# Performance work log

Measured on AMD Instinct MI355X. Metric: run time of the kernel, lower is better.

The kernel has to match this reference:

```python
import jax, jax.numpy as jnp
import numpy as np
import math

DIM_IN, DIM_CTX, DIM_KEY, DIM_VAL = 2048, 512, 128, 128
N, T, H, W = 8, 16, 32, 32
NBOX = 512


def setup_inputs() -> dict:
    key = jax.random.key(0)
    ks = jax.random.split(key, 10)
    rois = jax.random.normal(ks[0], (NBOX, DIM_IN), dtype=jnp.float32)
    context = jax.random.normal(ks[1], (N, DIM_CTX, T, H, W), dtype=jnp.float32)
    batch_idx = jnp.sort(jax.random.randint(ks[2], (NBOX,), 0, N))
    s = 0.02
    W_proj = jax.random.normal(ks[3], (DIM_KEY, DIM_IN), dtype=jnp.float32) * s
    b_proj = jnp.zeros((DIM_KEY,), dtype=jnp.float32)
    W_keys = jax.random.normal(ks[4], (DIM_KEY, DIM_CTX), dtype=jnp.float32) * s
    b_keys = jnp.zeros((DIM_KEY,), dtype=jnp.float32)
    W_vals = jax.random.normal(ks[5], (DIM_VAL, DIM_CTX), dtype=jnp.float32) * s
    b_vals = jnp.zeros((DIM_VAL,), dtype=jnp.float32)
    return {"rois": rois, "context": context, "batch_idx": batch_idx,
            "W_proj": W_proj, "b_proj": b_proj,
            "W_keys": W_keys, "b_keys": b_keys,
            "W_vals": W_vals, "b_vals": b_vals}


def reference(rois, context, batch_idx, W_proj, b_proj, W_keys, b_keys, W_vals, b_vals):
    n, c, t, h, w = context.shape
    s = t * h * w
    dk = W_keys.shape[0]
    # ROI query projection: [Nb, dk]
    q = rois @ W_proj.T + b_proj
    # 1x1x1 Conv3d == per-voxel linear over channels
    ctx_flat = context.reshape(n, c, s)                       # [N, C, S]
    keys = jnp.einsum('kc,ncs->nks', W_keys, ctx_flat) + b_keys[None, :, None]  # [N, dk, S]
    vals = jnp.einsum('vc,ncs->nsv', W_vals, ctx_flat) + b_vals[None, None, :]  # [N, S, dv]
    # Per-box gather of its clip's keys/vals, fused cross-attention
    qk = jnp.einsum('bk,bks->bs', q, keys[batch_idx]) / math.sqrt(dk)  # [Nb, S]
    coeff = jax.nn.softmax(qk, axis=-1)
    ctx_out = jnp.einsum('bs,bsv->bv', coeff, vals[batch_idx])         # [Nb, dv]
    attn = coeff.reshape(-1, t, h, w) * 255.0
    return ctx_out, attn
```

## Files before the change

kernel.cpp:

```cpp
#include <hip/hip_runtime.h>
#include <hip/hip_bf16.h>
#include <math.h>

#define DIM_IN  2048
#define DIM_CTX 512
#define DIM_KEY 128
#define DIM_VAL 128
#define NCLIP   8
#define S_TOT   16384
#define NBOX    512
#define MAXB    96

typedef __attribute__((ext_vector_type(8))) short short8_t;
typedef __attribute__((ext_vector_type(4))) float f32x4;

__device__ inline unsigned short f2bf(float x) {
    union { float f; unsigned int u; } v; v.f = x;
    unsigned int r = v.u + 0x7FFFu + ((v.u >> 16) & 1u);
    return (unsigned short)(r >> 16);
}
__device__ inline float bf2f(unsigned short h) {
    union { unsigned int u; float f; } v; v.u = ((unsigned int)h) << 16;
    return v.f;
}

__global__ __launch_bounds__(256) void k0_init(const int* __restrict__ batch_idx,
                                               int* __restrict__ ranges,
                                               float* __restrict__ cctx) {
    int idx = blockIdx.x * blockDim.x + threadIdx.x;
    for (int i = idx; i < NBOX * DIM_CTX; i += gridDim.x * blockDim.x)
        cctx[i] = 0.0f;
    if (blockIdx.x == 0) {
        __shared__ int s_start[NCLIP], s_end[NCLIP];
        if (threadIdx.x < NCLIP) { s_start[threadIdx.x] = NBOX; s_end[threadIdx.x] = 0; }
        __syncthreads();
        for (int i = threadIdx.x; i < NBOX; i += blockDim.x) {
            int b = batch_idx[i];
            atomicMin(&s_start[b], i);
            atomicMax(&s_end[b], i + 1);
        }
        __syncthreads();
        if (threadIdx.x < NCLIP) {
            ranges[threadIdx.x]         = s_start[threadIdx.x];
            ranges[NCLIP + threadIdx.x] = s_end[threadIdx.x];
        }
    }
}

__global__ __launch_bounds__(128) void k1a_q(const float* __restrict__ rois,
                                             const float* __restrict__ W_proj,
                                             const float* __restrict__ b_proj,
                                             float* __restrict__ q) {
    __shared__ float s_roi[4 * DIM_IN];
    int b0 = blockIdx.x * 4;
    const float4* src = (const float4*)(rois + (size_t)b0 * DIM_IN);
    for (int i = threadIdx.x; i < 4 * DIM_IN / 4; i += blockDim.x)
        ((float4*)s_roi)[i] = src[i];
    __syncthreads();
    int k = threadIdx.x;
    const float4* wrow = (const float4*)(W_proj + (size_t)k * DIM_IN);
    float a0 = 0.f, a1 = 0.f, a2 = 0.f, a3 = 0.f;
    for (int i = 0; i < DIM_IN / 4; ++i) {
        float4 w  = wrow[i];
        float4 r0 = *(const float4*)&s_roi[0 * DIM_IN + i * 4];
        float4 r1 = *(const float4*)&s_roi[1 * DIM_IN + i * 4];
        float4 r2 = *(const float4*)&s_roi[2 * DIM_IN + i * 4];
        float4 r3 = *(const float4*)&s_roi[3 * DIM_IN + i * 4];
        a0 += w.x * r0.x; a0 += w.y * r0.y; a0 += w.z * r0.z; a0 += w.w * r0.w;
        a1 += w.x * r1.x; a1 += w.y * r1.y; a1 += w.z * r1.z; a1 += w.w * r1.w;
        a2 += w.x * r2.x; a2 += w.y * r2.y; a2 += w.z * r2.z; a2 += w.w * r2.w;
        a3 += w.x * r3.x; a3 += w.y * r3.y; a3 += w.z * r3.z; a3 += w.w * r3.w;
    }
    float bp = b_proj[k];
    q[(size_t)(b0 + 0) * DIM_KEY + k] = a0 + bp;
    q[(size_t)(b0 + 1) * DIM_KEY + k] = a1 + bp;
    q[(size_t)(b0 + 2) * DIM_KEY + k] = a2 + bp;
    q[(size_t)(b0 + 3) * DIM_KEY + k] = a3 + bp;
}

__global__ __launch_bounds__(256) void k1b_qw(const float* __restrict__ q,
                                              const float* __restrict__ W_keys,
                                              const float* __restrict__ b_keys,
                                              unsigned short* __restrict__ qW_hi,
                                              unsigned short* __restrict__ qW_lo,
                                              float* __restrict__ qbias) {
    __shared__ float s_q[4 * DIM_KEY];
    __shared__ float red[256];
    int b0 = blockIdx.x * 4;
    for (int i = threadIdx.x; i < 4 * DIM_KEY; i += blockDim.x)
        s_q[i] = q[(size_t)b0 * DIM_KEY + i];
    __syncthreads();
    int c0 = threadIdx.x, c1 = threadIdx.x + 256;
    float a[4][2] = {{0.f,0.f},{0.f,0.f},{0.f,0.f},{0.f,0.f}};
    for (int k = 0; k < DIM_KEY; ++k) {
        float w0 = W_keys[(size_t)k * DIM_CTX + c0];
        float w1 = W_keys[(size_t)k * DIM_CTX + c1];
        float q0 = s_q[0 * DIM_KEY + k], q1 = s_q[1 * DIM_KEY + k];
        float q2 = s_q[2 * DIM_KEY + k], q3 = s_q[3 * DIM_KEY + k];
        a[0][0] += q0 * w0; a[0][1] += q0 * w1;
        a[1][0] += q1 * w0; a[1][1] += q1 * w1;
        a[2][0] += q2 * w0; a[2][1] += q2 * w1;
        a[3][0] += q3 * w0; a[3][1] += q3 * w1;
    }
    #pragma unroll
    for (int j = 0; j < 4; ++j) {
        #pragma unroll
        for (int cc = 0; cc < 2; ++cc) {
            int c = (cc == 0) ? c0 : c1;
            float x = a[j][cc];
            unsigned short h = f2bf(x);
            qW_hi[(size_t)(b0 + j) * DIM_CTX + c] = h;
            qW_lo[(size_t)(b0 + j) * DIM_CTX + c] = f2bf(x - bf2f(h));
        }
    }
    for (int j = 0; j < 4; ++j) {
        float v = 0.f;
        if (threadIdx.x < DIM_KEY) v = s_q[j * DIM_KEY + threadIdx.x] * b_keys[threadIdx.x];
        red[threadIdx.x] = v;
        __syncthreads();
        for (int st = 128; st > 0; st >>= 1) {
            if (threadIdx.x < st) red[threadIdx.x] += red[threadIdx.x + st];
            __syncthreads();
        }
        if (threadIdx.x == 0) qbias[b0 + j] = red[0];
        __syncthreads();
    }
}

__global__ __launch_bounds__(256) void k2_scores(
    const float* __restrict__ ctx, const unsigned short* __restrict__ qW_hi,
    const unsigned short* __restrict__ qW_lo, const float* __restrict__ qbias,
    const int* __restrict__ ranges, float* __restrict__ scores)
{
    int n = blockIdx.y;
    int start = ranges[n], Mb = ranges[NCLIP + n] - start;
    if (Mb <= 0) return;
    const float* ctxn = ctx + (size_t)n * DIM_CTX * S_TOT;
    int sch = blockIdx.x * 128;
    int t = threadIdx.x, lane = t & 63, w = t >> 6;

    __shared__ float          ls_f[32 * 132];
    __shared__ unsigned short ls_qh[MAXB * 32];
    __shared__ unsigned short ls_ql[MAXB * 32];
    __shared__ unsigned short ls_th[128 * 32];
    __shared__ unsigned short ls_tl[128 * 32];

    for (int bp = 0; bp < Mb; bp += MAXB) {
        int nb = min(MAXB, Mb - bp);
        f32x4 acc[6][2];
        #pragma unroll
        for (int m = 0; m < 6; ++m)
            #pragma unroll
            for (int nn = 0; nn < 2; ++nn)
                acc[m][nn] = (f32x4){0.f, 0.f, 0.f, 0.f};

        for (int ch = 0; ch < 16; ++ch) {
            int c0 = ch * 32;
            __syncthreads();
            #pragma unroll
            for (int rep = 0; rep < 4; ++rep) {
                int idx = t + rep * 256;
                int c_l = idx >> 5, s4 = (idx & 31) * 4;
                float4 v = *(const float4*)(ctxn + (size_t)(c0 + c_l) * S_TOT + sch + s4);
                *(float4*)&ls_f[c_l * 132 + s4] = v;
            }
            for (int idx = t; idx < MAXB * 4; idx += 256) {
                int row = idx >> 2, c8 = (idx & 3) * 8;
                uint4 vh = {0,0,0,0}, vl = {0,0,0,0};
                if (row < nb) {
                    size_t go = (size_t)(start + bp + row) * DIM_CTX + c0 + c8;
                    vh = *(const uint4*)(qW_hi + go);
                    vl = *(const uint4*)(qW_lo + go);
                }
                int off = (row * 64 + c8 * 2) ^ ((row & 7) << 4);
                *(uint4*)((char*)ls_qh + off) = vh;
                *(uint4*)((char*)ls_ql + off) = vl;
            }
            __syncthreads();
            {
                int s_l = t >> 1, c16 = (t & 1) * 16;
                unsigned short hb[16], lb[16];
                #pragma unroll
                for (int i = 0; i < 16; ++i) {
                    float x = ls_f[(c16 + i) * 132 + s_l];
                    unsigned short h = f2bf(x);
                    hb[i] = h;
                    lb[i] = f2bf(x - bf2f(h));
                }
                int base = s_l * 64 + c16 * 2;
                int sw = (s_l & 7) << 4;
                uint4 p0, p1, q0, q1;
                p0.x = hb[0] | ((unsigned)hb[1] << 16);  p0.y = hb[2] | ((unsigned)hb[3] << 16);
                p0.z = hb[4] | ((unsigned)hb[5] << 16);  p0.w = hb[6] | ((unsigned)hb[7] << 16);
                p1.x = hb[8] | ((unsigned)hb[9] << 16);  p1.y = hb[10] | ((unsigned)hb[11] << 16);
                p1.z = hb[12] | ((unsigned)hb[13] << 16); p1.w = hb[14] | ((unsigned)hb[15] << 16);
                q0.x = lb[0] | ((unsigned)lb[1] << 16);  q0.y = lb[2] | ((unsigned)lb[3] << 16);
                q0.z = lb[4] | ((unsigned)lb[5] << 16);  q0.w = lb[6] | ((unsigned)lb[7] << 16);
                q1.x = lb[8] | ((unsigned)lb[9] << 16);  q1.y = lb[10] | ((unsigned)lb[11] << 16);
                q1.z = lb[12] | ((unsigned)lb[13] << 16); q1.w = lb[14] | ((unsigned)lb[15] << 16);
                *(uint4*)((char*)ls_th + ((base)      ^ sw)) = p0;
                *(uint4*)((char*)ls_th + ((base + 16) ^ sw)) = p1;
                *(uint4*)((char*)ls_tl + ((base)      ^ sw)) = q0;
                *(uint4*)((char*)ls_tl + ((base + 16) ^ sw)) = q1;
            }
            __syncthreads();
            short8_t Ah[6], Al[6], Bh[2], Bl[2];
            int hi16 = (lane >> 4) * 16;
            #pragma unroll
            for (int m = 0; m < 6; ++m) {
                if (m * 16 < nb) {
                    int row = m * 16 + (lane & 15);
                    int off = (row * 64 + hi16) ^ ((row & 7) << 4);
                    Ah[m] = *(const short8_t*)((const char*)ls_qh + off);
                    Al[m] = *(const short8_t*)((const char*)ls_ql + off);
                }
            }
            #pragma unroll
            for (int nn = 0; nn < 2; ++nn) {
                int srow = (w * 2 + nn) * 16 + (lane & 15);
                int off = (srow * 64 + hi16) ^ ((srow & 7) << 4);
                Bh[nn] = *(const short8_t*)((const char*)ls_th + off);
                Bl[nn] = *(const short8_t*)((const char*)ls_tl + off);
            }
            #pragma unroll
            for (int m = 0; m < 6; ++m) {
                if (m * 16 < nb) {
                    #pragma unroll
                    for (int nn = 0; nn < 2; ++nn) {
                        acc[m][nn] = __builtin_amdgcn_mfma_f32_16x16x32_bf16(Ah[m], Bh[nn], acc[m][nn], 0, 0, 0);
                        acc[m][nn] = __builtin_amdgcn_mfma_f32_16x16x32_bf16(Ah[m], Bl[nn], acc[m][nn], 0, 0, 0);
                        acc[m][nn] = __builtin_amdgcn_mfma_f32_16x16x32_bf16(Al[m], Bh[nn], acc[m][nn], 0, 0, 0);
                    }
                }
            }
        }
        const float rs = 0.08838834764831845f;
        #pragma unroll
        for (int m = 0; m < 6; ++m)
            #pragma unroll
            for (int r = 0; r < 4; ++r) {
                int b_l = m * 16 + ((lane >> 4) << 2) + r;
                if (b_l < nb) {
                    int bg = start + bp + b_l;
                    float qb = qbias[bg];
                    #pragma unroll
                    for (int nn = 0; nn < 2; ++nn) {
                        int s = sch + (w * 2 + nn) * 16 + (lane & 15);
                        scores[(size_t)bg * S_TOT + s] = (acc[m][nn][r] + qb) * rs;
                    }
                }
            }
        __syncthreads();
    }
}

__global__ __launch_bounds__(256) void k3_stats(const float* __restrict__ scores,
                                                float* __restrict__ rmax,
                                                float* __restrict__ rsum) {
    int b = blockIdx.x;
    const float4* row = (const float4*)(scores + (size_t)b * S_TOT);
    __shared__ float red[256];
    float mx = -1e30f;
    for (int i = threadIdx.x; i < S_TOT / 4; i += 256) {
        float4 v = row[i];
        mx = fmaxf(mx, fmaxf(fmaxf(v.x, v.y), fmaxf(v.z, v.w)));
    }
    red[threadIdx.x] = mx;
    __syncthreads();
    for (int st = 128; st > 0; st >>= 1) {
        if (threadIdx.x < st) red[threadIdx.x] = fmaxf(red[threadIdx.x], red[threadIdx.x + st]);
        __syncthreads();
    }
    mx = red[0];
    __syncthreads();
    float sm = 0.f;
    for (int i = threadIdx.x; i < S_TOT / 4; i += 256) {
        float4 v = row[i];
        sm += __expf(v.x - mx) + __expf(v.y - mx) + __expf(v.z - mx) + __expf(v.w - mx);
    }
    red[threadIdx.x] = sm;
    __syncthreads();
    for (int st = 128; st > 0; st >>= 1) {
        if (threadIdx.x < st) red[threadIdx.x] += red[threadIdx.x + st];
        __syncthreads();
    }
    if (threadIdx.x == 0) { rmax[b] = mx; rsum[b] = 1.0f / red[0]; }
}

__global__ __launch_bounds__(256) void k4_pv(
    const float* __restrict__ ctx, const int* __restrict__ ranges,
    const float* __restrict__ rmax, const float* __restrict__ rsum,
    float* __restrict__ attn, float* __restrict__ cctx)
{
    int n = blockIdx.y;
    int start = ranges[n], Mb = ranges[NCLIP + n] - start;
    if (Mb <= 0) return;
    const float* ctxn = ctx + (size_t)n * DIM_CTX * S_TOT;
    int sch = blockIdx.x * 256;
    int t = threadIdx.x, lane = t & 63, w = t >> 6;
    int mh = w >> 1, ns = w & 1;

    __shared__ unsigned short ls_p[MAXB * 256];
    __shared__ unsigned short ls_c[32 * 256];

    for (int bp = 0; bp < Mb; bp += MAXB) {
        int nb = min(MAXB, Mb - bp);
        bool a0v = (mh + 0) * 16 < nb;
        bool a1v = (mh + 2) * 16 < nb;
        bool a2v = (mh + 4) * 16 < nb;
        __syncthreads();
        for (int idx = t; idx < MAXB * 64; idx += 256) {
            int b_l = idx >> 6, s4 = (idx & 63) * 4;
            uint2 pk; pk.x = 0u; pk.y = 0u;
            if (b_l < nb) {
                int bg = start + bp + b_l;
                size_t off = (size_t)bg * S_TOT + sch + s4;
                float4 v = *(const float4*)(attn + off);
                float m = rmax[bg], r = rsum[bg];
                float4 p;
                p.x = __expf(v.x - m) * r; p.y = __expf(v.y - m) * r;
                p.z = __expf(v.z - m) * r; p.w = __expf(v.w - m) * r;
                float4 o;
                o.x = 255.f * p.x; o.y = 255.f * p.y; o.z = 255.f * p.z; o.w = 255.f * p.w;
                *(float4*)(attn + off) = o;
                pk.x = f2bf(p.x) | ((unsigned)f2bf(p.y) << 16);
                pk.y = f2bf(p.z) | ((unsigned)f2bf(p.w) << 16);
            }
            int off8 = (b_l * 512 + s4 * 2) ^ ((b_l & 7) << 4);
            *(uint2*)((char*)ls_p + off8) = pk;
        }
        __syncthreads();
        short8_t A[3][8];
        int hi16 = (lane >> 4) * 16;
        #pragma unroll
        for (int mi = 0; mi < 3; ++mi) {
            int tm = mh + 2 * mi;
            if (tm * 16 < nb) {
                int row = tm * 16 + (lane & 15);
                int sw = (row & 7) << 4;
                #pragma unroll
                for (int k = 0; k < 8; ++k) {
                    int off = (row * 512 + k * 64 + hi16) ^ sw;
                    A[mi][k] = *(const short8_t*)((const char*)ls_p + off);
                }
            }
        }
        for (int ct = 0; ct < 16; ++ct) {
            __syncthreads();
            for (int idx = t; idx < 32 * 64; idx += 256) {
                int c_l = idx >> 6, s4 = (idx & 63) * 4;
                float4 v = *(const float4*)(ctxn + (size_t)(ct * 32 + c_l) * S_TOT + sch + s4);
                uint2 pk;
                pk.x = f2bf(v.x) | ((unsigned)f2bf(v.y) << 16);
                pk.y = f2bf(v.z) | ((unsigned)f2bf(v.w) << 16);
                int off8 = (c_l * 512 + s4 * 2) ^ ((c_l & 7) << 4);
                *(uint2*)((char*)ls_c + off8) = pk;
            }
            __syncthreads();
            f32x4 acc0 = (f32x4){0,0,0,0}, acc1 = (f32x4){0,0,0,0}, acc2 = (f32x4){0,0,0,0};
            int crow = ns * 16 + (lane & 15);
            int swc = (crow & 7) << 4;
            #pragma unroll
            for (int k = 0; k < 8; ++k) {
                int off = (crow * 512 + k * 64 + hi16) ^ swc;
                short8_t B = *(const short8_t*)((const char*)ls_c + off);
                if (a0v) acc0 = __builtin_amdgcn_mfma_f32_16x16x32_bf16(A[0][k], B, acc0, 0, 0, 0);
                if (a1v) acc1 = __builtin_amdgcn_mfma_f32_16x16x32_bf16(A[1][k], B, acc1, 0, 0, 0);
                if (a2v) acc2 = __builtin_amdgcn_mfma_f32_16x16x32_bf16(A[2][k], B, acc2, 0, 0, 0);
            }
            int cg = ct * 32 + ns * 16 + (lane & 15);
            #pragma unroll
            for (int r = 0; r < 4; ++r) {
                int br = ((lane >> 4) << 2) + r;
                int b0l = (mh + 0) * 16 + br;
                int b1l = (mh + 2) * 16 + br;
                int b2l = (mh + 4) * 16 + br;
                if (a0v && b0l < nb) atomicAdd(&cctx[(size_t)(start + bp + b0l) * DIM_CTX + cg], acc0[r]);
                if (a1v && b1l < nb) atomicAdd(&cctx[(size_t)(start + bp + b1l) * DIM_CTX + cg], acc1[r]);
                if (a2v && b2l < nb) atomicAdd(&cctx[(size_t)(start + bp + b2l) * DIM_CTX + cg], acc2[r]);
            }
        }
    }
}

__global__ __launch_bounds__(128) void k5_out(const float* __restrict__ cctx,
                                              const float* __restrict__ W_vals,
                                              const float* __restrict__ b_vals,
                                              float* __restrict__ out) {
    __shared__ float s_c[4 * DIM_CTX];
    int b0 = blockIdx.x * 4;
    const float4* src = (const float4*)(cctx + (size_t)b0 * DIM_CTX);
    for (int i = threadIdx.x; i < 4 * DIM_CTX / 4; i += blockDim.x)
        ((float4*)s_c)[i] = src[i];
    __syncthreads();
    int v = threadIdx.x;
    const float4* wrow = (const float4*)(W_vals + (size_t)v * DIM_CTX);
    float a0 = 0.f, a1 = 0.f, a2 = 0.f, a3 = 0.f;
    for (int i = 0; i < DIM_CTX / 4; ++i) {
        float4 w  = wrow[i];
        float4 c0v = *(const float4*)&s_c[0 * DIM_CTX + i * 4];
        float4 c1v = *(const float4*)&s_c[1 * DIM_CTX + i * 4];
        float4 c2v = *(const float4*)&s_c[2 * DIM_CTX + i * 4];
        float4 c3v = *(const float4*)&s_c[3 * DIM_CTX + i * 4];
        a0 += w.x * c0v.x; a0 += w.y * c0v.y; a0 += w.z * c0v.z; a0 += w.w * c0v.w;
        a1 += w.x * c1v.x; a1 += w.y * c1v.y; a1 += w.z * c1v.z; a1 += w.w * c1v.w;
        a2 += w.x * c2v.x; a2 += w.y * c2v.y; a2 += w.z * c2v.z; a2 += w.w * c2v.w;
        a3 += w.x * c3v.x; a3 += w.y * c3v.y; a3 += w.z * c3v.z; a3 += w.w * c3v.w;
    }
    float bb = b_vals[v];
    out[(size_t)(b0 + 0) * DIM_VAL + v] = a0 + bb;
    out[(size_t)(b0 + 1) * DIM_VAL + v] = a1 + bb;
    out[(size_t)(b0 + 2) * DIM_VAL + v] = a2 + bb;
    out[(size_t)(b0 + 3) * DIM_VAL + v] = a3 + bb;
}

extern "C" void kernel_launch(void* const* d_in, const int* in_sizes, int n_in,
                              void* d_out, int out_size, void* d_ws, size_t ws_size,
                              hipStream_t stream) {
    const float* rois      = (const float*)d_in[0];
    const float* context   = (const float*)d_in[1];
    const int*   batch_idx = (const int*)  d_in[2];
    const float* W_proj    = (const float*)d_in[3];
    const float* b_proj    = (const float*)d_in[4];
    const float* W_keys    = (const float*)d_in[5];
    const float* b_keys    = (const float*)d_in[6];
    const float* W_vals    = (const float*)d_in[7];
    const float* b_vals    = (const float*)d_in[8];

    float* out  = (float*)d_out;
    float* attn = out + NBOX * DIM_VAL;

    char* wsb = (char*)d_ws;
    int*   ranges = (int*)wsb;
    float* q      = (float*)(wsb + 128);
    float* qbias  = q + NBOX * DIM_KEY;
    float* rmaxp  = qbias + NBOX;
    float* rsump  = rmaxp + NBOX;
    float* cctx   = rsump + NBOX;
    unsigned short* qW_hi = (unsigned short*)(cctx + NBOX * DIM_CTX);
    unsigned short* qW_lo = qW_hi + NBOX * DIM_CTX;

    k0_init  <<<dim3(64),       dim3(256), 0, stream>>>(batch_idx, ranges, cctx);
    k1a_q    <<<dim3(NBOX / 4), dim3(128), 0, stream>>>(rois, W_proj, b_proj, q);
    k1b_qw   <<<dim3(NBOX / 4), dim3(256), 0, stream>>>(q, W_keys, b_keys, qW_hi, qW_lo, qbias);
    k2_scores<<<dim3(128, 8),   dim3(256), 0, stream>>>(context, qW_hi, qW_lo, qbias, ranges, attn);
    k3_stats <<<dim3(NBOX),     dim3(256), 0, stream>>>(attn, rmaxp, rsump);
    k4_pv    <<<dim3(64, 8),    dim3(256), 0, stream>>>(context, ranges, rmaxp, rsump, attn, cctx);
    k5_out   <<<dim3(NBOX / 4), dim3(128), 0, stream>>>(cctx, W_vals, b_vals, out);
}
```

Before: 645.7 us.

## Precompute bf16 context copies once, drop low-part split for scores

Adds a conversion kernel that reads the fp32 context once and writes both a channel-major bf16 copy and a transposed voxel-major bf16 copy. The scores kernel then loads pre-transposed bf16 tiles directly and drops the per-block fp32->bf16 hi/lo split, using two MFMA products instead of three. The PV kernel reads the bf16 copy instead of converting fp32. This removes repeated conversion work and halves context read bytes in the consumers, at the cost of an extra full pass writing 32MB of bf16 data and lower score precision on the context side.

```diff
diff --git a/kernel.cpp b/kernel.cpp
--- a/kernel.cpp
+++ b/kernel.cpp
@@ -45,6 +45,42 @@
             ranges[NCLIP + threadIdx.x] = s_end[threadIdx.x];
         }
     }
+}
+
+__global__ __launch_bounds__(256) void conv_ctx(const float* __restrict__ ctx,
+                                                unsigned short* __restrict__ ctxB,
+                                                unsigned short* __restrict__ ctxT) {
+    int n = blockIdx.z;
+    int c0 = blockIdx.y * 64;
+    int sch = blockIdx.x * 128;
+    int t = threadIdx.x;
+    __shared__ float ls[64 * 132];
+    const float* src = ctx + ((size_t)n * DIM_CTX + c0) * S_TOT + sch;
+    unsigned short* dstB = ctxB + ((size_t)n * DIM_CTX + c0) * S_TOT + sch;
+    #pragma unroll
+    for (int r = 0; r < 8; ++r) {
+        int idx = t + r * 256;
+        int c_l = idx >> 5, s4 = (idx & 31) * 4;
+        float4 v = *(const float4*)(src + (size_t)c_l * S_TOT + s4);
+        *(float4*)&ls[c_l * 132 + s4] = v;
+        uint2 pk;
+        pk.x = f2bf(v.x) | ((unsigned)f2bf(v.y) << 16);
+        pk.y = f2bf(v.z) | ((unsigned)f2bf(v.w) << 16);
+        *(uint2*)(dstB + (size_t)c_l * S_TOT + s4) = pk;
+    }
+    __syncthreads();
+    int s_l = t >> 1, ch = (t & 1) * 32;
+    unsigned int pk[16];
+    #pragma unroll
+    for (int i = 0; i < 16; ++i) {
+        unsigned short h0 = f2bf(ls[(ch + 2 * i + 0) * 132 + s_l]);
+        unsigned short h1 = f2bf(ls[(ch + 2 * i + 1) * 132 + s_l]);
+        pk[i] = h0 | ((unsigned)h1 << 16);
+    }
+    unsigned short* dstT = ctxT + ((size_t)n * S_TOT + sch + s_l) * DIM_CTX + c0 + ch;
+    #pragma unroll
+    for (int i = 0; i < 4; ++i)
+        ((uint4*)dstT)[i] = *(uint4*)&pk[i * 4];
 }
 
 __global__ __launch_bounds__(128) void k1a_q(const float* __restrict__ rois,
@@ -128,22 +164,20 @@
 }
 
 __global__ __launch_bounds__(256) void k2_scores(
-    const float* __restrict__ ctx, const unsigned short* __restrict__ qW_hi,
+    const unsigned short* __restrict__ ctxT, const unsigned short* __restrict__ qW_hi,
     const unsigned short* __restrict__ qW_lo, const float* __restrict__ qbias,
     const int* __restrict__ ranges, float* __restrict__ scores)
 {
     int n = blockIdx.y;
     int start = ranges[n], Mb = ranges[NCLIP + n] - start;
     if (Mb <= 0) return;
-    const float* ctxn = ctx + (size_t)n * DIM_CTX * S_TOT;
+    const unsigned short* ctxTn = ctxT + (size_t)n * S_TOT * DIM_CTX;
     int sch = blockIdx.x * 128;
     int t = threadIdx.x, lane = t & 63, w = t >> 6;
 
-    __shared__ float          ls_f[32 * 132];
-    __shared__ unsigned short ls_qh[MAXB * 32];
-    __shared__ unsigned short ls_ql[MAXB * 32];
-    __shared__ unsigned short ls_th[128 * 32];
-    __shared__ unsigned short ls_tl[128 * 32];
+    __shared__ unsigned short ls_b[128 * 64];
+    __shared__ unsigned short ls_qh[MAXB * 64];
+    __shared__ unsigned short ls_ql[MAXB * 64];
 
     for (int bp = 0; bp < Mb; bp += MAXB) {
         int nb = min(MAXB, Mb - bp);
@@ -154,82 +188,56 @@
             for (int nn = 0; nn < 2; ++nn)
                 acc[m][nn] = (f32x4){0.f, 0.f, 0.f, 0.f};
 
-        for (int ch = 0; ch < 16; ++ch) {
-            int c0 = ch * 32;
+        for (int it = 0; it < 8; ++it) {
+            int c0 = it * 64;
             __syncthreads();
             #pragma unroll
-            for (int rep = 0; rep < 4; ++rep) {
-                int idx = t + rep * 256;
-                int c_l = idx >> 5, s4 = (idx & 31) * 4;
-                float4 v = *(const float4*)(ctxn + (size_t)(c0 + c_l) * S_TOT + sch + s4);
-                *(float4*)&ls_f[c_l * 132 + s4] = v;
-            }
-            for (int idx = t; idx < MAXB * 4; idx += 256) {
-                int row = idx >> 2, c8 = (idx & 3) * 8;
+            for (int r = 0; r < 4; ++r) {
+                int idx = t + r * 256;
+                int s_l = idx >> 3, c8 = (idx & 7) * 8;
+                uint4 v = *(const uint4*)(ctxTn + (size_t)(sch + s_l) * DIM_CTX + c0 + c8);
+                *(uint4*)((char*)ls_b + ((s_l * 128 + c8 * 2) ^ ((s_l & 7) << 4))) = v;
+            }
+            for (int idx = t; idx < MAXB * 8; idx += 256) {
+                int row = idx >> 3, c8 = (idx & 7) * 8;
                 uint4 vh = {0,0,0,0}, vl = {0,0,0,0};
                 if (row < nb) {
                     size_t go = (size_t)(start + bp + row) * DIM_CTX + c0 + c8;
                     vh = *(const uint4*)(qW_hi + go);
                     vl = *(const uint4*)(qW_lo + go);
                 }
-                int off = (row * 64 + c8 * 2) ^ ((row & 7) << 4);
+                int off = (row * 128 + c8 * 2) ^ ((row & 7) << 4);
                 *(uint4*)((char*)ls_qh + off) = vh;
                 *(uint4*)((char*)ls_ql + off) = vl;
             }
             __syncthreads();
-            {
-                int s_l = t >> 1, c16 = (t & 1) * 16;
-                unsigned short hb[16], lb[16];
+            #pragma unroll
+            for (int ks = 0; ks < 2; ++ks) {
+                int hi16 = ks * 64 + (lane >> 4) * 16;
+                short8_t Ah[6], Al[6], Bv[2];
                 #pragma unroll
-                for (int i = 0; i < 16; ++i) {
-                    float x = ls_f[(c16 + i) * 132 + s_l];
-                    unsigned short h = f2bf(x);
-                    hb[i] = h;
-                    lb[i] = f2bf(x - bf2f(h));
-                }
-                int base = s_l * 64 + c16 * 2;
-                int sw = (s_l & 7) << 4;
-                uint4 p0, p1, q0, q1;
-                p0.x = hb[0] | ((unsigned)hb[1] << 16);  p0.y = hb[2] | ((unsigned)hb[3] << 16);
-                p0.z = hb[4] | ((unsigned)hb[5] << 16);  p0.w = hb[6] | ((unsigned)hb[7] << 16);
-                p1.x = hb[8] | ((unsigned)hb[9] << 16);  p1.y = hb[10] | ((unsigned)hb[11] << 16);
-                p1.z = hb[12] | ((unsigned)hb[13] << 16); p1.w = hb[14] | ((unsigned)hb[15] << 16);
-                q0.x = lb[0] | ((unsigned)lb[1] << 16);  q0.y = lb[2] | ((unsigned)lb[3] << 16);
-                q0.z = lb[4] | ((unsigned)lb[5] << 16);  q0.w = lb[6] | ((unsigned)lb[7] << 16);
-                q1.x = lb[8] | ((unsigned)lb[9] << 16);  q1.y = lb[10] | ((unsigned)lb[11] << 16);
-                q1.z = lb[12] | ((unsigned)lb[13] << 16); q1.w = lb[14] | ((unsigned)lb[15] << 16);
-                *(uint4*)((char*)ls_th + ((base)      ^ sw)) = p0;
-                *(uint4*)((char*)ls_th + ((base + 16) ^ sw)) = p1;
-                *(uint4*)((char*)ls_tl + ((base)      ^ sw)) = q0;
-                *(uint4*)((char*)ls_tl + ((base + 16) ^ sw)) = q1;
-            }
-            __syncthreads();
-            short8_t Ah[6], Al[6], Bh[2], Bl[2];
-            int hi16 = (lane >> 4) * 16;
-            #pragma unroll
-            for (int m = 0; m < 6; ++m) {
-                if (m * 16 < nb) {
-                    int row = m * 16 + (lane & 15);
-                    int off = (row * 64 + hi16) ^ ((row & 7) << 4);
-                    Ah[m] = *(const short8_t*)((const char*)ls_qh + off);
-                    Al[m] = *(const short8_t*)((const char*)ls_ql + off);
-                }
-            }
-            #pragma unroll
-            for (int nn = 0; nn < 2; ++nn) {
-                int srow = (w * 2 + nn) * 16 + (lane & 15);
-                int off = (srow * 64 + hi16) ^ ((srow & 7) << 4);
-                Bh[nn] = *(const short8_t*)((const char*)ls_th + off);
-                Bl[nn] = *(const short8_t*)((const char*)ls_tl + off);
-            }
-            #pragma unroll
-            for (int m = 0; m < 6; ++m) {
-                if (m * 16 < nb) {
-                    #pragma unroll
-                    for (int nn = 0; nn < 2; ++nn) {
-                        acc[m][nn] = __builtin_amdgcn_mfma_f32_16x16x32_bf16(Ah[m], Bh[nn], acc[m][nn], 0, 0, 0);
-                        acc[m][nn] = __builtin_amdgcn_mfma_f32_16x16x32_bf16(Ah[m], Bl[nn], acc[m][nn], 0, 0, 0);
-                        acc[m][nn] = __builtin_amdgcn_mfma_f32_16x16x32_bf16(Al[m], Bh[nn], acc[m][nn], 0, 0, 0);
+                for (int m = 0; m < 6; ++m) {
+                    if (m * 16 < nb) {
+                        int row = m * 16 + (lane & 15);
+                        int off = (row * 128 + hi16) ^ ((row & 7) << 4);
+                        Ah[m] = *(const short8_t*)((const char*)ls_qh + off);
+                        Al[m] = *(const short8_t*)((const char*)ls_ql + off);
+                    }
+                }
+                #pragma unroll
+                for (int nn = 0; nn < 2; ++nn) {
+                    int srow = (w * 2 + nn) * 16 + (lane & 15);
+                    int off = (srow * 128 + hi16) ^ ((srow & 7) << 4);
+                    Bv[nn] = *(const short8_t*)((const char*)ls_b + off);
+                }
+                #pragma unroll
+                for (int m = 0; m < 6; ++m) {
+                    if (m * 16 < nb) {
+                        #pragma unroll
+                        for (int nn = 0; nn < 2; ++nn) {
+                            acc[m][nn] = __builtin_amdgcn_mfma_f32_16x16x32_bf16(Ah[m], Bv[nn], acc[m][nn], 0, 0, 0);
+                            acc[m][nn] = __builtin_amdgcn_mfma_f32_16x16x32_bf16(Al[m], Bv[nn], acc[m][nn], 0, 0, 0);
+                        }
                     }
                 }
             }
@@ -288,14 +296,14 @@
 }
 
 __global__ __launch_bounds__(256) void k4_pv(
-    const float* __restrict__ ctx, const int* __restrict__ ranges,
+    const unsigned short* __restrict__ ctxB, const int* __restrict__ ranges,
     const float* __restrict__ rmax, const float* __restrict__ rsum,
     float* __restrict__ attn, float* __restrict__ cctx)
 {
     int n = blockIdx.y;
     int start = ranges[n], Mb = ranges[NCLIP + n] - start;
     if (Mb <= 0) return;
-    const float* ctxn = ctx + (size_t)n * DIM_CTX * S_TOT;
+    const unsigned short* ctxn = ctxB + (size_t)n * DIM_CTX * S_TOT;
     int sch = blockIdx.x * 256;
     int t = threadIdx.x, lane = t & 63, w = t >> 6;
     int mh = w >> 1, ns = w & 1;
@@ -347,14 +355,13 @@
         }
         for (int ct = 0; ct < 16; ++ct) {
             __syncthreads();
-            for (int idx = t; idx < 32 * 64; idx += 256) {
-                int c_l = idx >> 6, s4 = (idx & 63) * 4;
-                float4 v = *(const float4*)(ctxn + (size_t)(ct * 32 + c_l) * S_TOT + sch + s4);
-                uint2 pk;
-                pk.x = f2bf(v.x) | ((unsigned)f2bf(v.y) << 16);
-                pk.y = f2bf(v.z) | ((unsigned)f2bf(v.w) << 16);
-                int off8 = (c_l * 512 + s4 * 2) ^ ((c_l & 7) << 4);
-                *(uint2*)((char*)ls_c + off8) = pk;
+            #pragma unroll
+            for (int r = 0; r < 4; ++r) {
+                int idx = t + r * 256;
+                int c_l = idx >> 5, s8 = (idx & 31) * 8;
+                uint4 v = *(const uint4*)(ctxn + (size_t)(ct * 32 + c_l) * S_TOT + sch + s8);
+                int off8 = (c_l * 512 + s8 * 2) ^ ((c_l & 7) << 4);
+                *(uint4*)((char*)ls_c + off8) = v;
             }
             __syncthreads();
             f32x4 acc0 = (f32x4){0,0,0,0}, acc1 = (f32x4){0,0,0,0}, acc2 = (f32x4){0,0,0,0};
@@ -439,12 +446,15 @@
     float* cctx   = rsump + NBOX;
     unsigned short* qW_hi = (unsigned short*)(cctx + NBOX * DIM_CTX);
     unsigned short* qW_lo = qW_hi + NBOX * DIM_CTX;
-
-    k0_init  <<<dim3(64),       dim3(256), 0, stream>>>(batch_idx, ranges, cctx);
-    k1a_q    <<<dim3(NBOX / 4), dim3(128), 0, stream>>>(rois, W_proj, b_proj, q);
-    k1b_qw   <<<dim3(NBOX / 4), dim3(256), 0, stream>>>(q, W_keys, b_keys, qW_hi, qW_lo, qbias);
-    k2_scores<<<dim3(128, 8),   dim3(256), 0, stream>>>(context, qW_hi, qW_lo, qbias, ranges, attn);
-    k3_stats <<<dim3(NBOX),     dim3(256), 0, stream>>>(attn, rmaxp, rsump);
-    k4_pv    <<<dim3(64, 8),    dim3(256), 0, stream>>>(context, ranges, rmaxp, rsump, attn, cctx);
-    k5_out   <<<dim3(NBOX / 4), dim3(128), 0, stream>>>(cctx, W_vals, b_vals, out);
-}
+    unsigned short* ctxB  = qW_lo + NBOX * DIM_CTX;
+    unsigned short* ctxT  = ctxB + (size_t)NCLIP * DIM_CTX * S_TOT;
+
+    k0_init  <<<dim3(64),        dim3(256), 0, stream>>>(batch_idx, ranges, cctx);
+    conv_ctx <<<dim3(128, 8, 8), dim3(256), 0, stream>>>(context, ctxB, ctxT);
+    k1a_q    <<<dim3(NBOX / 4),  dim3(128), 0, stream>>>(rois, W_proj, b_proj, q);
+    k1b_qw   <<<dim3(NBOX / 4),  dim3(256), 0, stream>>>(q, W_keys, b_keys, qW_hi, qW_lo, qbias);
+    k2_scores<<<dim3(128, 8),    dim3(256), 0, stream>>>(ctxT, qW_hi, qW_lo, qbias, ranges, attn);
+    k3_stats <<<dim3(NBOX),      dim3(256), 0, stream>>>(attn, rmaxp, rsump);
+    k4_pv    <<<dim3(64, 8),     dim3(256), 0, stream>>>(ctxB, ranges, rmaxp, rsump, attn, cctx);
+    k5_out   <<<dim3(NBOX / 4),  dim3(128), 0, stream>>>(cctx, W_vals, b_vals, out);
+}
```

Measured after the change: 695.9 us. 7.8% more time.
